# Kernel optimization log

Hardware: AMD Instinct MI355X
Metric: run time of the kernel (lower is better)

## Reference

```python
import jax, jax.numpy as jnp
import numpy as np

D_MODEL = 1024
D_STATE = 16
D_CONV = 4
EXPAND = 2
D_INNER = EXPAND * D_MODEL          # 2048
DT_RANK = (D_MODEL + 15) // 16      # 64
B, L = 4, 2048


def setup_inputs() -> dict:
    key = jax.random.key(0)
    ks = jax.random.split(key, 10)
    s = 0.02
    x = jax.random.normal(ks[0], (B, L, D_MODEL), dtype=jnp.float32)
    # weights stored (in, out) so y = x @ W
    W_in = jax.random.normal(ks[1], (D_MODEL, 2 * D_INNER), dtype=jnp.float32) * s
    conv_w = jax.random.normal(ks[2], (D_INNER, D_CONV), dtype=jnp.float32) * 0.2
    conv_b = jnp.zeros((D_INNER,), dtype=jnp.float32)
    W_xproj = jax.random.normal(ks[3], (D_INNER, DT_RANK + 2 * D_STATE), dtype=jnp.float32) * s
    W_dt = jax.random.normal(ks[4], (DT_RANK, D_INNER), dtype=jnp.float32) * s
    b_dt = jax.random.uniform(ks[5], (D_INNER,), dtype=jnp.float32, minval=-4.0, maxval=-2.0)
    # S4D real init: A = -exp(A_log), A_log = log(1..d_state)
    A_log = jnp.log(jnp.broadcast_to(jnp.arange(1, D_STATE + 1, dtype=jnp.float32), (D_INNER, D_STATE)))
    Dp = jnp.ones((D_INNER,), dtype=jnp.float32)
    W_out = jax.random.normal(ks[6], (D_INNER, D_MODEL), dtype=jnp.float32) * s
    return {"x": x, "W_in": W_in, "conv_w": conv_w, "conv_b": conv_b,
            "W_xproj": W_xproj, "W_dt": W_dt, "b_dt": b_dt,
            "A_log": A_log, "Dp": Dp, "W_out": W_out}


def _causal_depthwise_conv(u, conv_w, conv_b):
    # u: (B, L, D_INNER); depthwise causal conv, kernel D_CONV
    uc = jnp.transpose(u, (0, 2, 1))                      # (B, D, L)
    k = conv_w[:, None, :]                                # (D, 1, K)
    y = jax.lax.conv_general_dilated(
        uc, k, window_strides=(1,), padding=[(D_CONV - 1, 0)],
        feature_group_count=D_INNER,
        dimension_numbers=('NCH', 'OIH', 'NCH'))
    y = y + conv_b[None, :, None]
    return jnp.transpose(y, (0, 2, 1))                    # (B, L, D)


def _selective_scan(u, delta, A, Bm, Cm, Dp):
    # u, delta: (B, L, d); A: (d, n); Bm, Cm: (B, L, n)
    def step(h, inp):
        u_t, dt_t, B_t, C_t = inp                         # (B,d),(B,d),(B,n),(B,n)
        dA = jnp.exp(dt_t[..., None] * A)                 # (B, d, n)
        h = h * dA + (dt_t * u_t)[..., None] * B_t[:, None, :]
        y = jnp.einsum('bdn,bn->bd', h, C_t)
        return h, y

    h0 = jnp.zeros((u.shape[0], u.shape[2], A.shape[1]), dtype=u.dtype)
    xs = (jnp.swapaxes(u, 0, 1), jnp.swapaxes(delta, 0, 1),
          jnp.swapaxes(Bm, 0, 1), jnp.swapaxes(Cm, 0, 1))
    _, ys = jax.lax.scan(step, h0, xs)
    y = jnp.swapaxes(ys, 0, 1)                            # (B, L, d)
    return y + u * Dp


def reference(x, W_in, conv_w, conv_b, W_xproj, W_dt, b_dt, A_log, Dp, W_out):
    xz = x @ W_in                                         # (B, L, 2*D_INNER)
    u, z = jnp.split(xz, 2, axis=-1)
    u = jax.nn.silu(_causal_depthwise_conv(u, conv_w, conv_b))
    proj = u @ W_xproj                                    # (B, L, DT_RANK + 2*D_STATE)
    dt_r = proj[..., :DT_RANK]
    Bm = proj[..., DT_RANK:DT_RANK + D_STATE]
    Cm = proj[..., DT_RANK + D_STATE:]
    delta = jax.nn.softplus(dt_r @ W_dt + b_dt)           # (B, L, D_INNER)
    A = -jnp.exp(A_log)                                   # (D_INNER, D_STATE)
    y = _selective_scan(u, delta, A, Bm, Cm, Dp)
    y = y * jax.nn.silu(z)
    return y @ W_out
```

## Files before the change

kernel.cpp:

```cpp
#include <hip/hip_runtime.h>
#include <hip/hip_bf16.h>
#include <math.h>

#define MTOK   8192
#define LSEQ   2048
#define NBATCH 4
#define DMODEL 1024
#define DINNER 2048
#define DSTATE 16
#define DTRANK 64
#define NXZ    4096
#define CHUNK  64
#define NCH    32
#define NPROJ  (MTOK * 96)
#define SPLITK 8

typedef _Float16 f16;
using f16x8 = __attribute__((ext_vector_type(8))) _Float16;
using f16x4 = __attribute__((ext_vector_type(4))) _Float16;
using f32x4 = __attribute__((ext_vector_type(4))) float;

__device__ __forceinline__ float silu_f(float x) { return x / (1.f + __expf(-x)); }

__device__ __forceinline__ void gload_lds16(const void* g, void* l) {
    __builtin_amdgcn_global_load_lds(
        (const __attribute__((address_space(1))) void*)g,
        (__attribute__((address_space(3))) void*)l, 16, 0, 0);
}

__global__ __launch_bounds__(256)
void cvt_f2h(const float* __restrict__ in, f16* __restrict__ out, int n4)
{
    const int i = blockIdx.x * 256 + threadIdx.x;
    if (i >= n4) return;
    const float4 v = ((const float4*)in)[i];
    f16x4 o;
    o[0] = (f16)v.x; o[1] = (f16)v.y; o[2] = (f16)v.z; o[3] = (f16)v.w;
    ((f16x4*)out)[i] = o;
}

__global__ __launch_bounds__(256)
void tcvt(const float* __restrict__ in, f16* __restrict__ out, int R, int C)
{
    __shared__ float t[32][33];
    const int c0 = blockIdx.x * 32, r0 = blockIdx.y * 32;
    const int tx = threadIdx.x & 31, ty = threadIdx.x >> 5;
    #pragma unroll
    for (int j = 0; j < 4; ++j)
        t[ty + 8 * j][tx] = in[(size_t)(r0 + ty + 8 * j) * C + c0 + tx];
    __syncthreads();
    #pragma unroll
    for (int j = 0; j < 4; ++j)
        out[(size_t)(c0 + ty + 8 * j) * R + r0 + tx] = (f16)t[tx][ty + 8 * j];
}

template<int EPI, typename OUT_T>
__global__ __launch_bounds__(256)
void hgemm128(const f16* __restrict__ A, int lda,
              const f16* __restrict__ Bt, int ldb,
              OUT_T* __restrict__ C, int ldc,
              int K, const float* __restrict__ bias,
              OUT_T* __restrict__ C2, int splitcol)
{
    __shared__ __align__(16) f16 As[2][128 * 32];
    __shared__ __align__(16) f16 Bs[2][128 * 32];

    const int tid  = threadIdx.x;
    const int lane = tid & 63, wave = tid >> 6;
    const int wr = wave >> 1, wc = wave & 1;
    const int row0 = blockIdx.x * 128;
    int col0 = blockIdx.y * 128;

    const int lrow = lane >> 2, lcol = (lane & 3) * 8;
    const f16* Agw = A  + (size_t)(row0 + wave * 32 + lrow) * lda + lcol;
    const f16* Bgw = Bt + (size_t)(col0 + wave * 32 + lrow) * ldb + lcol;
    const int ldsbase = (wave * 32) * 32;

    const int frow = lane & 15, fk = (lane >> 4) * 8;
    const int nt = K / 32;

    f32x4 acc[4][4] = {};

    #pragma unroll
    for (int r = 0; r < 2; ++r) {
        gload_lds16(Agw + (size_t)r * 16 * lda, &As[0][ldsbase + r * 16 * 32]);
        gload_lds16(Bgw + (size_t)r * 16 * ldb, &Bs[0][ldsbase + r * 16 * 32]);
    }

    int cur = 0;
    for (int kt = 0; kt < nt; ++kt) {
        __syncthreads();
        if (kt + 1 < nt) {
            const int k0 = (kt + 1) * 32;
            #pragma unroll
            for (int r = 0; r < 2; ++r) {
                gload_lds16(Agw + (size_t)r * 16 * lda + k0, &As[cur ^ 1][ldsbase + r * 16 * 32]);
                gload_lds16(Bgw + (size_t)r * 16 * ldb + k0, &Bs[cur ^ 1][ldsbase + r * 16 * 32]);
            }
        }
        f16x8 af[4], bf[4];
        #pragma unroll
        for (int m = 0; m < 4; ++m)
            af[m] = *(const f16x8*)&As[cur][(wr * 64 + m * 16 + frow) * 32 + fk];
        #pragma unroll
        for (int n = 0; n < 4; ++n)
            bf[n] = *(const f16x8*)&Bs[cur][(wc * 64 + n * 16 + frow) * 32 + fk];
        #pragma unroll
        for (int m = 0; m < 4; ++m)
            #pragma unroll
            for (int n = 0; n < 4; ++n)
                acc[m][n] = __builtin_amdgcn_mfma_f32_16x16x32_f16(af[m], bf[n], acc[m][n], 0, 0, 0);
        cur ^= 1;
    }

    OUT_T* Cw = C;
    if (C2 != nullptr && col0 >= splitcol) { Cw = C2; col0 -= splitcol; }

    const int rbase = row0 + wr * 64 + (lane >> 4) * 4;
    const int cbase = col0 + wc * 64 + (lane & 15);
    #pragma unroll
    for (int m = 0; m < 4; ++m) {
        #pragma unroll
        for (int n = 0; n < 4; ++n) {
            const int col = cbase + n * 16;
            #pragma unroll
            for (int r = 0; r < 4; ++r) {
                const int row = rbase + m * 16 + r;
                float tv = acc[m][n][r];
                if (EPI == 1) {
                    tv += bias[col];
                    tv = (tv > 20.f) ? tv : __logf(1.f + __expf(tv));
                }
                Cw[(size_t)row * ldc + col] = (OUT_T)tv;
            }
        }
    }
}

__global__ __launch_bounds__(256)
void hgemm_n96(const f16* __restrict__ A,
               const f16* __restrict__ Bt,
               float* __restrict__ part)
{
    __shared__ __align__(16) f16 As[128][40];
    __shared__ __align__(16) f16 Bs[96][40];

    const int tid = threadIdx.x, lane = tid & 63, wave = tid >> 6;
    const int row0 = blockIdx.x * 128;
    const int sk = blockIdx.y;
    const int kbase = sk * (DINNER / SPLITK);

    const int srow = tid >> 1, skoff = (tid & 1) * 16;
    const f16* Ag = A  + (size_t)(row0 + srow) * DINNER + kbase + skoff;
    const f16* Bg = Bt + (size_t)srow * DINNER + kbase + skoff;

    const int frow = lane & 15, fk = (lane >> 4) * 8;

    f32x4 acc[2][6] = {};

    for (int kk = 0; kk < DINNER / SPLITK; kk += 32) {
        const f16x8 a0 = *(const f16x8*)(Ag + kk);
        const f16x8 a1 = *(const f16x8*)(Ag + kk + 8);
        f16x8 b0 = {}, b1 = {};
        if (tid < 192) { b0 = *(const f16x8*)(Bg + kk); b1 = *(const f16x8*)(Bg + kk + 8); }
        __syncthreads();
        *(f16x8*)&As[srow][skoff]     = a0;
        *(f16x8*)&As[srow][skoff + 8] = a1;
        if (tid < 192) {
            *(f16x8*)&Bs[srow][skoff]     = b0;
            *(f16x8*)&Bs[srow][skoff + 8] = b1;
        }
        __syncthreads();

        f16x8 af[2], bf[6];
        #pragma unroll
        for (int m = 0; m < 2; ++m)
            af[m] = *(const f16x8*)&As[wave * 32 + m * 16 + frow][fk];
        #pragma unroll
        for (int n = 0; n < 6; ++n)
            bf[n] = *(const f16x8*)&Bs[n * 16 + frow][fk];
        #pragma unroll
        for (int m = 0; m < 2; ++m)
            #pragma unroll
            for (int n = 0; n < 6; ++n)
                acc[m][n] = __builtin_amdgcn_mfma_f32_16x16x32_f16(af[m], bf[n], acc[m][n], 0, 0, 0);
    }

    #pragma unroll
    for (int m = 0; m < 2; ++m)
        #pragma unroll
        for (int n = 0; n < 6; ++n) {
            const int col = n * 16 + (lane & 15);
            #pragma unroll
            for (int r = 0; r < 4; ++r) {
                const int row = row0 + wave * 32 + m * 16 + (lane >> 4) * 4 + r;
                part[((size_t)sk * MTOK + row) * 96 + col] = acc[m][n][r];
            }
        }
}

__global__ __launch_bounds__(256)
void reduce3(const float* __restrict__ part, float* __restrict__ proj,
             f16* __restrict__ projh)
{
    const int e = blockIdx.x * 256 + threadIdx.x;
    float s = 0.f;
    #pragma unroll
    for (int i = 0; i < SPLITK; ++i) s += part[(size_t)i * NPROJ + e];
    proj[e]  = s;
    projh[e] = (f16)s;
}

__global__ __launch_bounds__(256)
void conv_silu_kernel(const f16* __restrict__ uph,
                      const float* __restrict__ cw, const float* __restrict__ cb,
                      f16* __restrict__ uh)
{
    const int mt  = blockIdx.x;
    const int ml0 = mt * 8;
    const int l0  = ml0 & (LSEQ - 1);
    const int d   = threadIdx.x * 8;

    float w[8][4];
    #pragma unroll
    for (int c = 0; c < 8; ++c) {
        const float4 wv = *(const float4*)(cw + (size_t)(d + c) * 4);
        w[c][0] = wv.x; w[c][1] = wv.y; w[c][2] = wv.z; w[c][3] = wv.w;
    }
    float bias[8];
    {
        const float4 b0 = *(const float4*)(cb + d);
        const float4 b1 = *(const float4*)(cb + d + 4);
        bias[0] = b0.x; bias[1] = b0.y; bias[2] = b0.z; bias[3] = b0.w;
        bias[4] = b1.x; bias[5] = b1.y; bias[6] = b1.z; bias[7] = b1.w;
    }

    f16x8 r[11];
    if (l0 != 0) {
        #pragma unroll
        for (int i = 0; i < 11; ++i)
            r[i] = *(const f16x8*)(uph + (size_t)(ml0 - 3 + i) * DINNER + d);
    } else {
        r[0] = f16x8{}; r[1] = f16x8{}; r[2] = f16x8{};
        #pragma unroll
        for (int i = 3; i < 11; ++i)
            r[i] = *(const f16x8*)(uph + (size_t)(ml0 - 3 + i) * DINNER + d);
    }

    #pragma unroll
    for (int i = 0; i < 8; ++i) {
        f16x8 o;
        #pragma unroll
        for (int c = 0; c < 8; ++c) {
            float a = bias[c];
            #pragma unroll
            for (int j = 0; j < 4; ++j)
                a = fmaf((float)r[i + j][c], w[c][j], a);
            o[c] = (f16)silu_f(a);
        }
        *(f16x8*)(uh + (size_t)(ml0 + i) * DINNER + d) = o;
    }
}

__device__ __forceinline__ bool load_A(const float* __restrict__ A_log, int d,
                                       float* Av)
{
    #pragma unroll
    for (int n = 0; n < DSTATE; ++n)
        Av[n] = -__expf(A_log[(size_t)d * DSTATE + n]);
    bool p = true;
    #pragma unroll
    for (int n = 1; n < DSTATE; ++n) {
        const float r = Av[n] / Av[0];
        if (fabsf(r - (float)(n + 1)) > 1e-3f) p = false;
    }
    return p;
}

__global__ __launch_bounds__(256)
void scan_pass1(const f16* __restrict__ uh,
                const f16* __restrict__ deltah,
                const float* __restrict__ proj,
                const float* __restrict__ A_log,
                float* __restrict__ Sbuf, float* __restrict__ sumdt)
{
    const int d = blockIdx.x * 256 + threadIdx.x;
    const int c = blockIdx.y;
    const int b = blockIdx.z;

    float Av[DSTATE];
    const bool pw = load_A(A_log, d, Av);
    const float Av0 = Av[0];

    __shared__ __align__(16) float Bsh[CHUNK][DSTATE];
    const float* projb = proj + ((size_t)b * LSEQ + (size_t)c * CHUNK) * 96;
    #pragma unroll
    for (int i = 0; i < (CHUNK * DSTATE) / 256; ++i) {
        const int f = i * 256 + threadIdx.x;
        Bsh[f >> 4][f & 15] = projb[(size_t)(f >> 4) * 96 + 64 + (f & 15)];
    }
    __syncthreads();

    float S[DSTATE];
    #pragma unroll
    for (int n = 0; n < DSTATE; ++n) S[n] = 0.f;
    float sdt = 0.f;

    const size_t tok0 = (size_t)b * LSEQ + (size_t)c * CHUNK;
    if (pw) {
        for (int l = 0; l < CHUNK; ++l) {
            const float dt = (float)deltah[(tok0 + l) * DINNER + d];
            const float uu = (float)uh[(tok0 + l) * DINNER + d];
            sdt += dt;
            const float du = dt * uu;
            const float p1 = __expf(dt * Av0);
            const float p2 = p1 * p1;
            const float p3 = p2 * p1;
            const float p4 = p2 * p2;
            float m = 1.f;
            #pragma unroll
            for (int g = 0; g < 4; ++g) {
                const f32x4 bb = *(const f32x4*)&Bsh[l][g * 4];
                S[g*4+0] = fmaf(S[g*4+0], m * p1, du * bb[0]);
                S[g*4+1] = fmaf(S[g*4+1], m * p2, du * bb[1]);
                S[g*4+2] = fmaf(S[g*4+2], m * p3, du * bb[2]);
                S[g*4+3] = fmaf(S[g*4+3], m * p4, du * bb[3]);
                m *= p4;
            }
        }
    } else {
        for (int l = 0; l < CHUNK; ++l) {
            const float dt = (float)deltah[(tok0 + l) * DINNER + d];
            const float uu = (float)uh[(tok0 + l) * DINNER + d];
            sdt += dt;
            const float du = dt * uu;
            #pragma unroll
            for (int n = 0; n < DSTATE; ++n)
                S[n] = fmaf(S[n], __expf(dt * Av[n]), du * Bsh[l][n]);
        }
    }

    const size_t base = (size_t)b * NCH + c;
    #pragma unroll
    for (int n = 0; n < DSTATE; ++n)
        Sbuf[(base * DSTATE + n) * DINNER + d] = S[n];
    sumdt[base * DINNER + d] = sdt;
}

__global__ __launch_bounds__(256)
void scan_pass2(const float* __restrict__ A_log,
                const float* __restrict__ sumdt,
                float* __restrict__ Sbuf)
{
    const int d = blockIdx.x * 256 + threadIdx.x;
    const int b = blockIdx.y;

    float Av[DSTATE];
    const bool pw = load_A(A_log, d, Av);
    const float Av0 = Av[0];

    float h[DSTATE];
    #pragma unroll
    for (int n = 0; n < DSTATE; ++n) h[n] = 0.f;

    for (int c = 0; c < NCH; ++c) {
        const size_t base = (size_t)b * NCH + c;
        const float sdt = sumdt[base * DINNER + d];
        if (pw) {
            const float p1 = __expf(sdt * Av0);
            const float p2 = p1 * p1;
            const float p3 = p2 * p1;
            const float p4 = p2 * p2;
            float m = 1.f;
            #pragma unroll
            for (int g = 0; g < 4; ++g) {
                const float pj[4] = {p1, p2, p3, p4};
                #pragma unroll
                for (int j = 0; j < 4; ++j) {
                    const int n = g * 4 + j;
                    const size_t idx = (base * DSTATE + n) * DINNER + d;
                    const float tmp = Sbuf[idx];
                    Sbuf[idx] = h[n];
                    h[n] = fmaf(h[n], m * pj[j], tmp);
                }
                m *= p4;
            }
        } else {
            #pragma unroll
            for (int n = 0; n < DSTATE; ++n) {
                const size_t idx = (base * DSTATE + n) * DINNER + d;
                const float tmp = Sbuf[idx];
                Sbuf[idx] = h[n];
                h[n] = fmaf(h[n], __expf(sdt * Av[n]), tmp);
            }
        }
    }
}

__global__ __launch_bounds__(256)
void scan_pass3(const f16* __restrict__ uh,
                const f16* __restrict__ deltah,
                const f16* __restrict__ zh,
                const float* __restrict__ proj,
                const float* __restrict__ A_log,
                const float* __restrict__ Dp,
                const float* __restrict__ Sbuf,
                f16* __restrict__ ygh)
{
    const int d = blockIdx.x * 256 + threadIdx.x;
    const int c = blockIdx.y;
    const int b = blockIdx.z;

    float Av[DSTATE];
    const bool pw = load_A(A_log, d, Av);
    const float Av0 = Av[0];

    float h[DSTATE];
    const size_t base = (size_t)b * NCH + c;
    #pragma unroll
    for (int n = 0; n < DSTATE; ++n)
        h[n] = Sbuf[(base * DSTATE + n) * DINNER + d];

    const float Dval = Dp[d];

    __shared__ __align__(16) float Bsh[CHUNK][DSTATE];
    __shared__ __align__(16) float Csh[CHUNK][DSTATE];
    const float* projb = proj + ((size_t)b * LSEQ + (size_t)c * CHUNK) * 96;
    #pragma unroll
    for (int i = 0; i < (CHUNK * 2 * DSTATE) / 256; ++i) {
        const int f = i * 256 + threadIdx.x;
        const int r = f >> 5, col = f & 31;
        const float v = projb[(size_t)r * 96 + 64 + col];
        if (col < DSTATE) Bsh[r][col] = v;
        else              Csh[r][col - DSTATE] = v;
    }
    __syncthreads();

    const size_t tok0 = (size_t)b * LSEQ + (size_t)c * CHUNK;
    for (int l = 0; l < CHUNK; ++l) {
        const size_t tok = tok0 + l;
        const float dt = (float)deltah[tok * DINNER + d];
        const float uu = (float)uh[tok * DINNER + d];
        const float zz = (float)zh[tok * DINNER + d];
        const float du = dt * uu;
        float y = 0.f;
        if (pw) {
            const float p1 = __expf(dt * Av0);
            const float p2 = p1 * p1;
            const float p3 = p2 * p1;
            const float p4 = p2 * p2;
            float m = 1.f;
            #pragma unroll
            for (int g = 0; g < 4; ++g) {
                const f32x4 bb = *(const f32x4*)&Bsh[l][g * 4];
                const f32x4 cc = *(const f32x4*)&Csh[l][g * 4];
                h[g*4+0] = fmaf(h[g*4+0], m * p1, du * bb[0]);
                h[g*4+1] = fmaf(h[g*4+1], m * p2, du * bb[1]);
                h[g*4+2] = fmaf(h[g*4+2], m * p3, du * bb[2]);
                h[g*4+3] = fmaf(h[g*4+3], m * p4, du * bb[3]);
                y = fmaf(h[g*4+0], cc[0], y);
                y = fmaf(h[g*4+1], cc[1], y);
                y = fmaf(h[g*4+2], cc[2], y);
                y = fmaf(h[g*4+3], cc[3], y);
                m *= p4;
            }
        } else {
            #pragma unroll
            for (int n = 0; n < DSTATE; ++n) {
                h[n] = fmaf(h[n], __expf(dt * Av[n]), du * Bsh[l][n]);
                y = fmaf(h[n], Csh[l][n], y);
            }
        }
        const float yt = fmaf(uu, Dval, y);
        ygh[tok * DINNER + d] = (f16)(yt * silu_f(zz));
    }
}

extern "C" void kernel_launch(void* const* d_in, const int* in_sizes, int n_in,
                              void* d_out, int out_size, void* d_ws, size_t ws_size,
                              hipStream_t stream)
{
    const float* x     = (const float*)d_in[0];
    const float* W_in  = (const float*)d_in[1];
    const float* cw    = (const float*)d_in[2];
    const float* cb    = (const float*)d_in[3];
    const float* W_xp  = (const float*)d_in[4];
    const float* W_dt  = (const float*)d_in[5];
    const float* b_dt  = (const float*)d_in[6];
    const float* A_log = (const float*)d_in[7];
    const float* Dp    = (const float*)d_in[8];
    const float* W_out = (const float*)d_in[9];
    float* out = (float*)d_out;

    float* updelta = (float*)d_ws;
    f16*   zh      = (f16*)(updelta + (size_t)MTOK * DINNER);
    f16*   uh      = zh + (size_t)MTOK * DINNER;
    float* proj    = (float*)(uh + (size_t)MTOK * DINNER);
    f16*   projh   = (f16*)(proj + NPROJ);
    float* Sbuf    = (float*)(projh + NPROJ);
    float* sumdt   = Sbuf + (size_t)NBATCH * NCH * DSTATE * DINNER;
    f16*   WxpT    = (f16*)(sumdt + (size_t)NBATCH * NCH * DINNER);
    f16*   WdtT    = WxpT + (size_t)96 * DINNER;
    f16*   WoutT   = WdtT + (size_t)DINNER * DTRANK;
    f16*   big     = WoutT + (size_t)DMODEL * DINNER;
    f16*   WinT    = big;
    float* part3   = (float*)(big + (size_t)NXZ * DMODEL);
    f16*   ygh     = big;
    f16*   xh      = uh;
    f16*   uph     = (f16*)updelta;
    f16*   deltah  = (f16*)updelta;

    cvt_f2h<<<(MTOK * DMODEL / 4 + 255) / 256, 256, 0, stream>>>(x, xh, MTOK * DMODEL / 4);
    tcvt<<<dim3(NXZ / 32, DMODEL / 32), 256, 0, stream>>>(W_in, WinT, DMODEL, NXZ);

    hgemm128<0, f16><<<dim3(64, 32), 256, 0, stream>>>(
        xh, DMODEL, WinT, DMODEL, uph, DINNER, DMODEL, nullptr, zh, DINNER);

    conv_silu_kernel<<<MTOK / 8, 256, 0, stream>>>(uph, cw, cb, uh);

    tcvt<<<dim3(96 / 32, DINNER / 32), 256, 0, stream>>>(W_xp, WxpT, DINNER, 96);
    hgemm_n96<<<dim3(64, SPLITK), 256, 0, stream>>>(uh, WxpT, part3);
    reduce3<<<NPROJ / 256, 256, 0, stream>>>(part3, proj, projh);

    tcvt<<<dim3(DINNER / 32, DTRANK / 32), 256, 0, stream>>>(W_dt, WdtT, DTRANK, DINNER);
    hgemm128<1, f16><<<dim3(64, 16), 256, 0, stream>>>(
        projh, 96, WdtT, DTRANK, deltah, DINNER, DTRANK, b_dt, nullptr, 0);

    scan_pass1<<<dim3(DINNER / 256, NCH, NBATCH), 256, 0, stream>>>(
        uh, deltah, proj, A_log, Sbuf, sumdt);
    scan_pass2<<<dim3(DINNER / 256, NBATCH), 256, 0, stream>>>(A_log, sumdt, Sbuf);
    scan_pass3<<<dim3(DINNER / 256, NCH, NBATCH), 256, 0, stream>>>(
        uh, deltah, zh, proj, A_log, Dp, Sbuf, ygh);

    tcvt<<<dim3(DMODEL / 32, DINNER / 32), 256, 0, stream>>>(W_out, WoutT, DINNER, DMODEL);
    hgemm128<0, float><<<dim3(64, 8), 256, 0, stream>>>(
        ygh, DINNER, WoutT, DINNER, out, DMODEL, DINNER, nullptr, nullptr, 0);
}
```

Baseline: 325.7 us.

## Replace in-projection GEMM with 256x256-tile triple-buffered 8-wave kernel

Adds a new hgemm256 kernel for the x@W_in projection. It uses 256x256 output tiles, 512 threads, triple-buffered LDS filled by direct global-to-LDS loads, and split A/B staging interleaved with MFMA phases under s_setprio. The goal is more data reuse per tile and better overlap of global loads with compute on the largest GEMM. In exchange it launches only 512 blocks, holds a large accumulator footprint at one block per CU, and lacks bounds checks.

```diff
diff --git a/kernel.cpp b/kernel.cpp
--- a/kernel.cpp
+++ b/kernel.cpp
@@ -28,6 +28,12 @@
         (__attribute__((address_space(3))) void*)l, 16, 0, 0);
 }
 
+__device__ __forceinline__ void barrier_sync() {
+    asm volatile("" ::: "memory");
+    __builtin_amdgcn_s_barrier();
+    asm volatile("" ::: "memory");
+}
+
 __global__ __launch_bounds__(256)
 void cvt_f2h(const float* __restrict__ in, f16* __restrict__ out, int n4)
 {
@@ -52,6 +58,109 @@
     #pragma unroll
     for (int j = 0; j < 4; ++j)
         out[(size_t)(c0 + ty + 8 * j) * R + r0 + tx] = (f16)t[tx][ty + 8 * j];
+}
+
+__global__ __launch_bounds__(512, 1)
+void hgemm256(const f16* __restrict__ A, int lda,
+              const f16* __restrict__ Bt, int ldb,
+              f16* __restrict__ C, int ldc,
+              int K, f16* __restrict__ C2, int splitcol)
+{
+    __shared__ __align__(16) f16 S[3][2][8192];
+
+    const int tid  = threadIdx.x;
+    const int lane = tid & 63, w = tid >> 6;
+    const int wr = w >> 2, wc = w & 3;
+    const int row0 = blockIdx.x * 256;
+    int col0 = blockIdx.y * 256;
+
+    const int srow = (w & 3) * 64 + lane;
+    const int scb  = w >> 2;
+    const f16* Asrc = A  + (size_t)(row0 + srow) * lda;
+    const f16* Bsrc = Bt + (size_t)(col0 + srow) * ldb;
+
+    const int frow = lane & 15;
+    const int g16  = lane >> 4;
+    const int nt = K / 32;
+
+    f32x4 acc[8][4] = {};
+
+    auto stageA = [&](int t) {
+        f16* dst = &S[t % 3][0][0];
+        #pragma unroll
+        for (int i = 0; i < 2; ++i)
+            gload_lds16(Asrc + t * 32 + (i * 2 + scb) * 8,
+                        dst + (size_t)(i * 512 + w * 64) * 8);
+    };
+    auto stageB = [&](int t) {
+        f16* dst = &S[t % 3][1][0];
+        #pragma unroll
+        for (int i = 0; i < 2; ++i)
+            gload_lds16(Bsrc + t * 32 + (i * 2 + scb) * 8,
+                        dst + (size_t)(i * 512 + w * 64) * 8);
+    };
+
+    stageA(0); stageB(0);
+    stageA(1); stageB(1);
+    asm volatile("s_waitcnt vmcnt(4)" ::: "memory");
+    barrier_sync();
+
+    for (int t = 0; t < nt; ++t) {
+        const f16* __restrict__ Al = &S[t % 3][0][0];
+        const f16* __restrict__ Bl = &S[t % 3][1][0];
+        f16x8 af[8], bf[4];
+
+        #pragma unroll
+        for (int m = 0; m < 4; ++m)
+            af[m] = *(const f16x8*)&Al[(size_t)(g16 * 256 + wr * 128 + m * 16 + frow) * 8];
+        #pragma unroll
+        for (int n = 0; n < 4; ++n)
+            bf[n] = *(const f16x8*)&Bl[(size_t)(g16 * 256 + wc * 64 + n * 16 + frow) * 8];
+        if (t + 2 < nt) stageA(t + 2);
+        barrier_sync();
+        __builtin_amdgcn_s_setprio(1);
+        #pragma unroll
+        for (int m = 0; m < 4; ++m)
+            #pragma unroll
+            for (int n = 0; n < 4; ++n)
+                acc[m][n] = __builtin_amdgcn_mfma_f32_16x16x32_f16(af[m], bf[n], acc[m][n], 0, 0, 0);
+        __builtin_amdgcn_s_setprio(0);
+        barrier_sync();
+
+        #pragma unroll
+        for (int m = 0; m < 4; ++m)
+            af[4 + m] = *(const f16x8*)&Al[(size_t)(g16 * 256 + wr * 128 + (m + 4) * 16 + frow) * 8];
+        if (t + 2 < nt) stageB(t + 2);
+        barrier_sync();
+        __builtin_amdgcn_s_setprio(1);
+        #pragma unroll
+        for (int m = 4; m < 8; ++m)
+            #pragma unroll
+            for (int n = 0; n < 4; ++n)
+                acc[m][n] = __builtin_amdgcn_mfma_f32_16x16x32_f16(af[m], bf[n], acc[m][n], 0, 0, 0);
+        __builtin_amdgcn_s_setprio(0);
+        if (t + 1 < nt) {
+            if (t + 2 < nt) asm volatile("s_waitcnt vmcnt(4)" ::: "memory");
+            else            asm volatile("s_waitcnt vmcnt(0)" ::: "memory");
+        }
+        barrier_sync();
+    }
+
+    f16* Cw = C;
+    if (C2 != nullptr && col0 >= splitcol) { Cw = C2; col0 -= splitcol; }
+
+    const int rbase = row0 + wr * 128 + (lane >> 4) * 4;
+    const int cbase = col0 + wc * 64 + (lane & 15);
+    #pragma unroll
+    for (int m = 0; m < 8; ++m) {
+        #pragma unroll
+        for (int n = 0; n < 4; ++n) {
+            const int col = cbase + n * 16;
+            #pragma unroll
+            for (int r = 0; r < 4; ++r)
+                Cw[(size_t)(rbase + m * 16 + r) * ldc + col] = (f16)acc[m][n][r];
+        }
+    }
 }
 
 template<int EPI, typename OUT_T>
@@ -513,8 +622,8 @@
     cvt_f2h<<<(MTOK * DMODEL / 4 + 255) / 256, 256, 0, stream>>>(x, xh, MTOK * DMODEL / 4);
     tcvt<<<dim3(NXZ / 32, DMODEL / 32), 256, 0, stream>>>(W_in, WinT, DMODEL, NXZ);
 
-    hgemm128<0, f16><<<dim3(64, 32), 256, 0, stream>>>(
-        xh, DMODEL, WinT, DMODEL, uph, DINNER, DMODEL, nullptr, zh, DINNER);
+    hgemm256<<<dim3(32, 16), 512, 0, stream>>>(
+        xh, DMODEL, WinT, DMODEL, uph, DINNER, DMODEL, zh, DINNER);
 
     conv_silu_kernel<<<MTOK / 8, 256, 0, stream>>>(uph, cw, cb, uh);
 
```

Result: no change. 326.2 us (+0.2%).
